# Performance work log

Hardware: AMD Instinct MI355X
Metric: run time of the kernel (lower is better)

The kernel has to match this reference:

```python
import jax, jax.numpy as jnp
import numpy as np

BOOST_STRENGTH = 1.0  # init kwarg boostStrength (already >= 0)


def setup_inputs() -> dict:
    key = jax.random.key(0)
    k1, k2 = jax.random.split(key)
    x = jax.random.normal(k1, (8192, 4096), dtype=jnp.float32)
    # duty cycles are running fractions of activity, roughly around k/n
    dutyCycles = jax.random.uniform(k2, (4096,), dtype=jnp.float32) * 0.2
    return {"x": x, "dutyCycles": dutyCycles, "k": 409}


def reference(x, dutyCycles, k):
    n = x.shape[1]
    boost_strength = jnp.maximum(jnp.float32(BOOST_STRENGTH), 0.0)
    target_density = jnp.float32(k) / jnp.float32(n)
    # boostFactors = exp[(targetDensity - dutyCycle) * boostStrength]
    boost_factors = jnp.exp((target_density - dutyCycles) * boost_strength)  # [n]
    boosted = x * boost_factors  # [B, n]
    topk_vals, _ = jax.lax.top_k(boosted, k)  # [B, k]
    bottom = jnp.min(topk_vals, axis=1, keepdims=True)  # per-row k-th largest
    mask = (boosted >= bottom).astype(x.dtype)
    return x * mask
```

## Files before the change

### kernel.cpp

```cpp
#include <hip/hip_runtime.h>
#include <cstdint>
#include <cstddef>

#define N_COLS 4096
#define TPB 256
#define NCOPY 8
#define HSTR 12
#define NHWORDS (256 * HSTR)
#define SURV_CAP 64

__global__ void boost_kernel(const float* __restrict__ dc,
                             const int* __restrict__ kp,
                             float* __restrict__ bf) {
    int i = blockIdx.x * blockDim.x + threadIdx.x;
    if (i < N_COLS) {
        float td = (float)kp[0] / (float)N_COLS;
        float arg = td - dc[i];
        bf[i] = (float)exp((double)arg);
    }
}

__device__ __forceinline__ uint32_t orderable(uint32_t u) {
    return (u & 0x80000000u) ? ~u : (u | 0x80000000u);
}

__global__ __launch_bounds__(TPB) void kwinner_kernel(
    const float* __restrict__ x, const float* __restrict__ bf,
    const int* __restrict__ kp, float* __restrict__ out)
{
    __shared__ uint32_t s_hist[NHWORDS];
    __shared__ uint32_t s_cnt[256];
    __shared__ uint32_t s_cand[SURV_CAP];
    __shared__ uint32_t s_m2;

    const int tid  = threadIdx.x;
    const int lane = tid & 63;
    const uint32_t copy = (uint32_t)(tid & (NCOPY - 1));
    const size_t row = blockIdx.x;
    const float4* xr = (const float4*)(x + row * (size_t)N_COLS);
    const float4* br = (const float4*)bf;
    float4* orow = (float4*)(out + row * (size_t)N_COLS);

    float4 xv[4];
    float xb[16];
    #pragma unroll
    for (int j = 0; j < 4; ++j) {
        float4 v = xr[tid + j * TPB];
        float4 b = br[tid + j * TPB];
        xv[j] = v;
        xb[j * 4 + 0] = v.x * b.x;
        xb[j * 4 + 1] = v.y * b.y;
        xb[j * 4 + 2] = v.z * b.z;
        xb[j * 4 + 3] = v.w * b.w;
    }

    {
        uint4* h4 = (uint4*)s_hist;
        uint4 z; z.x = z.y = z.z = z.w = 0u;
        #pragma unroll
        for (int j = 0; j < 3; ++j) h4[tid + j * TPB] = z;
    }
    if (tid == 0) s_m2 = 0;
    __syncthreads();

    const float T0f = 1.10f;
    #pragma unroll
    for (int e = 0; e < 16; ++e) {
        if (xb[e] >= T0f) {
            uint32_t d = (__float_as_uint(xb[e]) >> 16) - 0x3F80u;
            d = d > 255u ? 255u : d;
            atomicAdd(&s_hist[d * HSTR + copy], 1u);
        }
    }
    __syncthreads();

    const uint32_t k = (uint32_t)kp[0];
    uint32_t rem = k;

    uint32_t dsel;
    uint32_t packed;
    {
        uint32_t vv[4];
        const uint32_t b0 = (uint32_t)lane * 4u;
        #pragma unroll
        for (int i = 0; i < 4; ++i) {
            uint4 a  = *(const uint4*)&s_hist[(b0 + i) * HSTR];
            uint4 b2 = *(const uint4*)&s_hist[(b0 + i) * HSTR + 4];
            vv[i] = a.x + a.y + a.z + a.w + b2.x + b2.y + b2.z + b2.w;
        }
        uint32_t s3 = vv[3], s2 = vv[2] + s3, s1 = vv[1] + s2, s0 = vv[0] + s1;
        uint32_t T = s0;
        #pragma unroll
        for (int off = 1; off < 64; off <<= 1) {
            uint32_t t = (uint32_t)__shfl_down((int)T, off, 64);
            if (lane + off < 64) T += t;
        }
        uint32_t Tex = T - s0;
        uint32_t S0 = Tex + s0, S1 = Tex + s1, S2 = Tex + s2, S3 = Tex + s3;
        int b = -1; uint32_t sn = 0;
        if (S3 >= rem)      { b = 3; sn = S3 - vv[3]; }
        else if (S2 >= rem) { b = 2; sn = S2 - vv[2]; }
        else if (S1 >= rem) { b = 1; sn = S1 - vv[1]; }
        else if (S0 >= rem) { b = 0; sn = S0 - vv[0]; }
        packed = (b >= 0) ? ((((uint32_t)(4 * lane + b + 1)) << 16) | sn) : 0u;
        #pragma unroll
        for (int off = 1; off < 64; off <<= 1) {
            uint32_t o = (uint32_t)__shfl_xor((int)packed, off, 64);
            packed = packed > o ? packed : o;
        }
        dsel = (packed >> 16) - 1u;
        rem -= (packed & 0xFFFFu);
    }

    float thr = 0.0f;
    bool need_fallback = (packed == 0u) || (dsel == 255u);

    if (!need_fallback) {
        const uint32_t hi16 = 0x3F80u + dsel;
        #pragma unroll
        for (int e = 0; e < 16; ++e) {
            uint32_t ub = __float_as_uint(xb[e]);
            if ((ub >> 16) == hi16) {
                uint32_t pos = atomicAdd(&s_m2, 1u);
                if (pos < SURV_CAP) s_cand[pos] = ub;
            }
        }
        __syncthreads();
        const uint32_t m2 = s_m2;
        if (m2 <= SURV_CAP) {
            uint32_t cv = ((uint32_t)lane < m2) ? s_cand[lane] : ((~hi16) << 16);
            uint32_t cur = 0;
            #pragma unroll
            for (int bpos = 15; bpos >= 0; --bpos) {
                uint32_t t  = (hi16 << 16) | cur | (1u << bpos);
                uint32_t mk = ~((1u << bpos) - 1u);
                uint32_t c  = (uint32_t)__popcll(__ballot(((cv ^ t) & mk) == 0u));
                if (c >= rem) cur |= (1u << bpos);
                else          rem -= c;
            }
            thr = __uint_as_float((hi16 << 16) | cur);
        } else {
            need_fallback = true;
        }
    }

    if (need_fallback) {
        __syncthreads();
        {
            uint4* h4 = (uint4*)s_hist;
            uint4 z; z.x = z.y = z.z = z.w = 0u;
            #pragma unroll
            for (int j = 0; j < 3; ++j) h4[tid + j * TPB] = z;
        }
        __syncthreads();
        uint32_t prefix = 0;
        rem = k;
        const uint32_t pmasks[4] = {0u, 0xFF000000u, 0xFFFF0000u, 0xFFFFFF00u};
        #pragma unroll 1
        for (int pass = 0; pass < 4; ++pass) {
            const int shift = 24 - pass * 8;
            const uint32_t pm = pmasks[pass];
            #pragma unroll
            for (int e = 0; e < 16; ++e) {
                uint32_t ou = orderable(__float_as_uint(xb[e]));
                if (((ou ^ prefix) & pm) == 0u)
                    atomicAdd(&s_hist[((ou >> shift) & 255u) * HSTR + copy], 1u);
            }
            __syncthreads();
            {
                uint4 a  = *(const uint4*)&s_hist[tid * HSTR];
                uint4 b2 = *(const uint4*)&s_hist[tid * HSTR + 4];
                uint4 z; z.x = z.y = z.z = z.w = 0u;
                *(uint4*)&s_hist[tid * HSTR]     = z;
                *(uint4*)&s_hist[tid * HSTR + 4] = z;
                s_cnt[tid] = a.x + a.y + a.z + a.w + b2.x + b2.y + b2.z + b2.w;
            }
            __syncthreads();
            uint4 v = ((const uint4*)s_cnt)[lane];
            uint32_t s3 = v.w, s2 = v.z + s3, s1 = v.y + s2, s0 = v.x + s1;
            uint32_t T = s0;
            #pragma unroll
            for (int off = 1; off < 64; off <<= 1) {
                uint32_t t = (uint32_t)__shfl_down((int)T, off, 64);
                if (lane + off < 64) T += t;
            }
            uint32_t Tex = T - s0;
            uint32_t S0 = Tex + s0, S1 = Tex + s1, S2 = Tex + s2, S3 = Tex + s3;
            int b = -1; uint32_t sn = 0;
            if (S3 >= rem)      { b = 3; sn = S3 - v.w; }
            else if (S2 >= rem) { b = 2; sn = S2 - v.z; }
            else if (S1 >= rem) { b = 1; sn = S1 - v.y; }
            else if (S0 >= rem) { b = 0; sn = S0 - v.x; }
            uint32_t pk = (b >= 0) ? ((((uint32_t)(4 * lane + b + 1)) << 16) | sn) : 0u;
            #pragma unroll
            for (int off = 1; off < 64; off <<= 1) {
                uint32_t o = (uint32_t)__shfl_xor((int)pk, off, 64);
                pk = pk > o ? pk : o;
            }
            prefix |= ((pk >> 16) - 1u) << shift;
            rem -= (pk & 0xFFFFu);
        }
        uint32_t tu = (prefix & 0x80000000u) ? (prefix & 0x7FFFFFFFu) : ~prefix;
        thr = __uint_as_float(tu);
    }

    #pragma unroll
    for (int j = 0; j < 4; ++j) {
        float4 o;
        o.x = (xb[j * 4 + 0] >= thr) ? xv[j].x : 0.0f;
        o.y = (xb[j * 4 + 1] >= thr) ? xv[j].y : 0.0f;
        o.z = (xb[j * 4 + 2] >= thr) ? xv[j].z : 0.0f;
        o.w = (xb[j * 4 + 3] >= thr) ? xv[j].w : 0.0f;
        orow[tid + j * TPB] = o;
    }
}

extern "C" void kernel_launch(void* const* d_in, const int* in_sizes, int n_in,
                              void* d_out, int out_size, void* d_ws, size_t ws_size,
                              hipStream_t stream) {
    const float* x  = (const float*)d_in[0];
    const float* dc = (const float*)d_in[1];
    const int*   kp = (const int*)d_in[2];
    float* out = (float*)d_out;
    float* bf  = (float*)d_ws;

    const int n    = in_sizes[1];
    const int rows = in_sizes[0] / n;

    boost_kernel<<<(n + TPB - 1) / TPB, TPB, 0, stream>>>(dc, kp, bf);
    kwinner_kernel<<<rows, TPB, 0, stream>>>(x, bf, kp, out);
}
```

Baseline: 231.2 us.

## Process four rows per block with next-row prefetch and copy-major histogram

Each block now handles four rows and loads the next row's data into registers while the current row is being selected, so global load latency overlaps the histogram and scan work. The boost factors are loaded once per block and reused across its rows. The histogram layout changes from bin-major to copy-major with a padded stride, which changes the LDS access pattern for the reduction. Barriers become explicit lgkmcnt waits plus s_barrier. The cost is fewer blocks (2048 instead of 8192) and higher register pressure from the double-buffered rows.

```diff
diff --git a/kernel.cpp b/kernel.cpp
--- a/kernel.cpp
+++ b/kernel.cpp
@@ -4,10 +4,13 @@
 
 #define N_COLS 4096
 #define TPB 256
+#define RPB 4
 #define NCOPY 8
-#define HSTR 12
-#define NHWORDS (256 * HSTR)
+#define CSTR 260
+#define NHWORDS (NCOPY * CSTR)
 #define SURV_CAP 64
+
+static_assert(NHWORDS % 4 == 0, "hist must be uint4-clearable");
 
 __global__ void boost_kernel(const float* __restrict__ dc,
                              const int* __restrict__ kp,
@@ -24,44 +27,40 @@
     return (u & 0x80000000u) ? ~u : (u | 0x80000000u);
 }
 
-__global__ __launch_bounds__(TPB) void kwinner_kernel(
-    const float* __restrict__ x, const float* __restrict__ bf,
-    const int* __restrict__ kp, float* __restrict__ out)
+__device__ __forceinline__ void bar_lgkm() {
+    asm volatile("s_waitcnt lgkmcnt(0)\n\ts_barrier" ::: "memory");
+}
+
+template<bool PREF>
+__device__ __forceinline__ void process_row(
+    const float4* __restrict__ xpref, float4 (&xv)[4], float4 (&xn)[4],
+    const float4 (&bfv)[4], float4* __restrict__ orow, uint32_t k,
+    uint32_t* __restrict__ s_hist, uint32_t* __restrict__ s_cnt,
+    uint32_t* __restrict__ s_cand, uint32_t* __restrict__ s_m2,
+    int tid, int lane, uint32_t copy)
 {
-    __shared__ uint32_t s_hist[NHWORDS];
-    __shared__ uint32_t s_cnt[256];
-    __shared__ uint32_t s_cand[SURV_CAP];
-    __shared__ uint32_t s_m2;
-
-    const int tid  = threadIdx.x;
-    const int lane = tid & 63;
-    const uint32_t copy = (uint32_t)(tid & (NCOPY - 1));
-    const size_t row = blockIdx.x;
-    const float4* xr = (const float4*)(x + row * (size_t)N_COLS);
-    const float4* br = (const float4*)bf;
-    float4* orow = (float4*)(out + row * (size_t)N_COLS);
-
-    float4 xv[4];
-    float xb[16];
-    #pragma unroll
-    for (int j = 0; j < 4; ++j) {
-        float4 v = xr[tid + j * TPB];
-        float4 b = br[tid + j * TPB];
-        xv[j] = v;
-        xb[j * 4 + 0] = v.x * b.x;
-        xb[j * 4 + 1] = v.y * b.y;
-        xb[j * 4 + 2] = v.z * b.z;
-        xb[j * 4 + 3] = v.w * b.w;
-    }
-
+    if constexpr (PREF) {
+        #pragma unroll
+        for (int j = 0; j < 4; ++j) xn[j] = xpref[tid + j * TPB];
+    }
+
+    bar_lgkm();
     {
         uint4* h4 = (uint4*)s_hist;
         uint4 z; z.x = z.y = z.z = z.w = 0u;
-        #pragma unroll
-        for (int j = 0; j < 3; ++j) h4[tid + j * TPB] = z;
-    }
-    if (tid == 0) s_m2 = 0;
-    __syncthreads();
+        for (int w = tid; w < NHWORDS / 4; w += TPB) h4[w] = z;
+    }
+    if (tid == 0) *s_m2 = 0u;
+    bar_lgkm();
+
+    float xb[16];
+    #pragma unroll
+    for (int j = 0; j < 4; ++j) {
+        xb[j * 4 + 0] = xv[j].x * bfv[j].x;
+        xb[j * 4 + 1] = xv[j].y * bfv[j].y;
+        xb[j * 4 + 2] = xv[j].z * bfv[j].z;
+        xb[j * 4 + 3] = xv[j].w * bfv[j].w;
+    }
 
     const float T0f = 1.10f;
     #pragma unroll
@@ -69,26 +68,21 @@
         if (xb[e] >= T0f) {
             uint32_t d = (__float_as_uint(xb[e]) >> 16) - 0x3F80u;
             d = d > 255u ? 255u : d;
-            atomicAdd(&s_hist[d * HSTR + copy], 1u);
-        }
-    }
-    __syncthreads();
-
-    const uint32_t k = (uint32_t)kp[0];
+            atomicAdd(&s_hist[copy * CSTR + d], 1u);
+        }
+    }
+    bar_lgkm();
+
     uint32_t rem = k;
-
-    uint32_t dsel;
-    uint32_t packed;
+    uint32_t dsel, packed;
     {
-        uint32_t vv[4];
-        const uint32_t b0 = (uint32_t)lane * 4u;
-        #pragma unroll
-        for (int i = 0; i < 4; ++i) {
-            uint4 a  = *(const uint4*)&s_hist[(b0 + i) * HSTR];
-            uint4 b2 = *(const uint4*)&s_hist[(b0 + i) * HSTR + 4];
-            vv[i] = a.x + a.y + a.z + a.w + b2.x + b2.y + b2.z + b2.w;
-        }
-        uint32_t s3 = vv[3], s2 = vv[2] + s3, s1 = vv[1] + s2, s0 = vv[0] + s1;
+        uint32_t vv0 = 0, vv1 = 0, vv2 = 0, vv3 = 0;
+        #pragma unroll
+        for (int c = 0; c < NCOPY; ++c) {
+            uint4 a = *(const uint4*)&s_hist[c * CSTR + 4 * lane];
+            vv0 += a.x; vv1 += a.y; vv2 += a.z; vv3 += a.w;
+        }
+        uint32_t s3 = vv3, s2 = vv2 + s3, s1 = vv1 + s2, s0 = vv0 + s1;
         uint32_t T = s0;
         #pragma unroll
         for (int off = 1; off < 64; off <<= 1) {
@@ -98,10 +92,10 @@
         uint32_t Tex = T - s0;
         uint32_t S0 = Tex + s0, S1 = Tex + s1, S2 = Tex + s2, S3 = Tex + s3;
         int b = -1; uint32_t sn = 0;
-        if (S3 >= rem)      { b = 3; sn = S3 - vv[3]; }
-        else if (S2 >= rem) { b = 2; sn = S2 - vv[2]; }
-        else if (S1 >= rem) { b = 1; sn = S1 - vv[1]; }
-        else if (S0 >= rem) { b = 0; sn = S0 - vv[0]; }
+        if (S3 >= rem)      { b = 3; sn = S3 - vv3; }
+        else if (S2 >= rem) { b = 2; sn = S2 - vv2; }
+        else if (S1 >= rem) { b = 1; sn = S1 - vv1; }
+        else if (S0 >= rem) { b = 0; sn = S0 - vv0; }
         packed = (b >= 0) ? ((((uint32_t)(4 * lane + b + 1)) << 16) | sn) : 0u;
         #pragma unroll
         for (int off = 1; off < 64; off <<= 1) {
@@ -121,12 +115,12 @@
         for (int e = 0; e < 16; ++e) {
             uint32_t ub = __float_as_uint(xb[e]);
             if ((ub >> 16) == hi16) {
-                uint32_t pos = atomicAdd(&s_m2, 1u);
+                uint32_t pos = atomicAdd(s_m2, 1u);
                 if (pos < SURV_CAP) s_cand[pos] = ub;
             }
         }
-        __syncthreads();
-        const uint32_t m2 = s_m2;
+        bar_lgkm();
+        const uint32_t m2 = *s_m2;
         if (m2 <= SURV_CAP) {
             uint32_t cv = ((uint32_t)lane < m2) ? s_cand[lane] : ((~hi16) << 16);
             uint32_t cur = 0;
@@ -145,14 +139,13 @@
     }
 
     if (need_fallback) {
-        __syncthreads();
+        bar_lgkm();
         {
             uint4* h4 = (uint4*)s_hist;
             uint4 z; z.x = z.y = z.z = z.w = 0u;
-            #pragma unroll
-            for (int j = 0; j < 3; ++j) h4[tid + j * TPB] = z;
-        }
-        __syncthreads();
+            for (int w = tid; w < NHWORDS / 4; w += TPB) h4[w] = z;
+        }
+        bar_lgkm();
         uint32_t prefix = 0;
         rem = k;
         const uint32_t pmasks[4] = {0u, 0xFF000000u, 0xFFFF0000u, 0xFFFFFF00u};
@@ -164,18 +157,19 @@
             for (int e = 0; e < 16; ++e) {
                 uint32_t ou = orderable(__float_as_uint(xb[e]));
                 if (((ou ^ prefix) & pm) == 0u)
-                    atomicAdd(&s_hist[((ou >> shift) & 255u) * HSTR + copy], 1u);
-            }
-            __syncthreads();
+                    atomicAdd(&s_hist[copy * CSTR + ((ou >> shift) & 255u)], 1u);
+            }
+            bar_lgkm();
             {
-                uint4 a  = *(const uint4*)&s_hist[tid * HSTR];
-                uint4 b2 = *(const uint4*)&s_hist[tid * HSTR + 4];
-                uint4 z; z.x = z.y = z.z = z.w = 0u;
-                *(uint4*)&s_hist[tid * HSTR]     = z;
-                *(uint4*)&s_hist[tid * HSTR + 4] = z;
-                s_cnt[tid] = a.x + a.y + a.z + a.w + b2.x + b2.y + b2.z + b2.w;
-            }
-            __syncthreads();
+                uint32_t sum = 0;
+                #pragma unroll
+                for (int c = 0; c < NCOPY; ++c) {
+                    sum += s_hist[c * CSTR + tid];
+                    s_hist[c * CSTR + tid] = 0u;
+                }
+                s_cnt[tid] = sum;
+            }
+            bar_lgkm();
             uint4 v = ((const uint4*)s_cnt)[lane];
             uint32_t s3 = v.w, s2 = v.z + s3, s1 = v.y + s2, s0 = v.x + s1;
             uint32_t T = s0;
@@ -215,6 +209,51 @@
     }
 }
 
+__global__ __launch_bounds__(TPB) void kwinner_kernel(
+    const float* __restrict__ x, const float* __restrict__ bf,
+    const int* __restrict__ kp, float* __restrict__ out, int rows)
+{
+    __shared__ __align__(16) uint32_t s_hist[NHWORDS];
+    __shared__ uint32_t s_cnt[256];
+    __shared__ uint32_t s_cand[SURV_CAP];
+    __shared__ uint32_t s_m2;
+
+    const int tid  = threadIdx.x;
+    const int lane = tid & 63;
+    const uint32_t copy = (uint32_t)(tid & (NCOPY - 1));
+    const uint32_t k = (uint32_t)kp[0];
+
+    size_t r0 = (size_t)blockIdx.x * RPB;
+    size_t r1 = r0 + 1, r2 = r0 + 2, r3 = r0 + 3;
+    const size_t rmax = (size_t)rows - 1;
+    if (r0 > rmax) r0 = rmax;
+    if (r1 > rmax) r1 = rmax;
+    if (r2 > rmax) r2 = rmax;
+    if (r3 > rmax) r3 = rmax;
+
+    const float4* br = (const float4*)bf;
+    float4 bfv[4];
+    #pragma unroll
+    for (int j = 0; j < 4; ++j) bfv[j] = br[tid + j * TPB];
+
+    const size_t s4 = N_COLS / 4;
+    const float4* xg = (const float4*)x;
+    float4* og = (float4*)out;
+
+    float4 xA[4], xB[4];
+    #pragma unroll
+    for (int j = 0; j < 4; ++j) xA[j] = xg[r0 * s4 + tid + j * TPB];
+
+    process_row<true >(xg + r1 * s4, xA, xB, bfv, og + r0 * s4, k,
+                       s_hist, s_cnt, s_cand, &s_m2, tid, lane, copy);
+    process_row<true >(xg + r2 * s4, xB, xA, bfv, og + r1 * s4, k,
+                       s_hist, s_cnt, s_cand, &s_m2, tid, lane, copy);
+    process_row<true >(xg + r3 * s4, xA, xB, bfv, og + r2 * s4, k,
+                       s_hist, s_cnt, s_cand, &s_m2, tid, lane, copy);
+    process_row<false>(xg,           xB, xA, bfv, og + r3 * s4, k,
+                       s_hist, s_cnt, s_cand, &s_m2, tid, lane, copy);
+}
+
 extern "C" void kernel_launch(void* const* d_in, const int* in_sizes, int n_in,
                               void* d_out, int out_size, void* d_ws, size_t ws_size,
                               hipStream_t stream) {
@@ -228,5 +267,6 @@
     const int rows = in_sizes[0] / n;
 
     boost_kernel<<<(n + TPB - 1) / TPB, TPB, 0, stream>>>(dc, kp, bf);
-    kwinner_kernel<<<rows, TPB, 0, stream>>>(x, bf, kp, out);
-}
+    const int nb = (rows + RPB - 1) / RPB;
+    kwinner_kernel<<<nb, TPB, 0, stream>>>(x, bf, kp, out, rows);
+}
```

Result: slower. 245.5 us (+6.2%).

## Process one row per wavefront with wave-local histograms and LDS-staged boost factors

Applied to the files above, without the earlier changes.

Each 64-lane wavefront now owns a whole row: 16 float4 per lane, a private two-copy histogram, and private candidate buffers. Block-wide __syncthreads are replaced by wave-local lgkmcnt waits. Boost factors are staged once per block in LDS and the boosted products are recomputed from it instead of being held in registers. This removes block barriers and cross-wave histogram reduction, at the cost of more registers per lane, more LDS atomic contention within a wave, and relying on wave-synchronous LDS ordering.

```diff
diff --git a/kernel.cpp b/kernel.cpp
--- a/kernel.cpp
+++ b/kernel.cpp
@@ -4,9 +4,8 @@
 
 #define N_COLS 4096
 #define TPB 256
-#define NCOPY 8
-#define HSTR 12
-#define NHWORDS (256 * HSTR)
+#define WPB 4
+#define HSTRW 260
 #define SURV_CAP 64
 
 __global__ void boost_kernel(const float* __restrict__ dc,
@@ -24,71 +23,77 @@
     return (u & 0x80000000u) ? ~u : (u | 0x80000000u);
 }
 
-__global__ __launch_bounds__(TPB) void kwinner_kernel(
+__device__ __forceinline__ void wave_lgkm() {
+    asm volatile("s_waitcnt lgkmcnt(0)" ::: "memory");
+}
+
+__global__ __launch_bounds__(TPB, 4) void kwinner_kernel(
     const float* __restrict__ x, const float* __restrict__ bf,
-    const int* __restrict__ kp, float* __restrict__ out)
+    const int* __restrict__ kp, float* __restrict__ out, int rows)
 {
-    __shared__ uint32_t s_hist[NHWORDS];
-    __shared__ uint32_t s_cnt[256];
-    __shared__ uint32_t s_cand[SURV_CAP];
-    __shared__ uint32_t s_m2;
+    __shared__ __align__(16) float    s_bf[N_COLS];
+    __shared__ __align__(16) uint32_t s_hist[WPB][2][HSTRW];
+    __shared__ uint32_t s_cand[WPB][SURV_CAP];
+    __shared__ uint32_t s_m2[WPB * 8];
 
     const int tid  = threadIdx.x;
+    const int w    = tid >> 6;
     const int lane = tid & 63;
-    const uint32_t copy = (uint32_t)(tid & (NCOPY - 1));
-    const size_t row = blockIdx.x;
-    const float4* xr = (const float4*)(x + row * (size_t)N_COLS);
-    const float4* br = (const float4*)bf;
-    float4* orow = (float4*)(out + row * (size_t)N_COLS);
-
-    float4 xv[4];
-    float xb[16];
+
+    {
+        const float4* br = (const float4*)bf;
+        float4* sb = (float4*)s_bf;
+        #pragma unroll
+        for (int j = 0; j < 4; ++j) sb[tid + j * TPB] = br[tid + j * TPB];
+    }
+    __syncthreads();
+
+    size_t row = (size_t)blockIdx.x * WPB + (size_t)w;
+    const size_t rmax = (size_t)rows - 1;
+    if (row > rmax) row = rmax;
+
+    const float4* xr   = (const float4*)(x + row * (size_t)N_COLS);
+    float4*       orow = (float4*)(out + row * (size_t)N_COLS);
+    const float4* bf4  = (const float4*)s_bf;
+
+    float4 xv[16];
     #pragma unroll
-    for (int j = 0; j < 4; ++j) {
-        float4 v = xr[tid + j * TPB];
-        float4 b = br[tid + j * TPB];
-        xv[j] = v;
-        xb[j * 4 + 0] = v.x * b.x;
-        xb[j * 4 + 1] = v.y * b.y;
-        xb[j * 4 + 2] = v.z * b.z;
-        xb[j * 4 + 3] = v.w * b.w;
-    }
+    for (int jj = 0; jj < 16; ++jj) xv[jj] = xr[lane + 64 * jj];
+
+    uint32_t* hist = &s_hist[w][0][0];
+    uint32_t* m2p  = &s_m2[w * 8];
 
     {
-        uint4* h4 = (uint4*)s_hist;
         uint4 z; z.x = z.y = z.z = z.w = 0u;
-        #pragma unroll
-        for (int j = 0; j < 3; ++j) h4[tid + j * TPB] = z;
-    }
-    if (tid == 0) s_m2 = 0;
-    __syncthreads();
-
+        *(uint4*)&hist[4 * lane]         = z;
+        *(uint4*)&hist[HSTRW + 4 * lane] = z;
+        if (lane == 0) *m2p = 0u;
+    }
+    wave_lgkm();
+
+    const uint32_t cofs = (uint32_t)(lane & 1) * HSTRW;
     const float T0f = 1.10f;
     #pragma unroll
-    for (int e = 0; e < 16; ++e) {
-        if (xb[e] >= T0f) {
-            uint32_t d = (__float_as_uint(xb[e]) >> 16) - 0x3F80u;
-            d = d > 255u ? 255u : d;
-            atomicAdd(&s_hist[d * HSTR + copy], 1u);
-        }
-    }
-    __syncthreads();
+    for (int jj = 0; jj < 16; ++jj) {
+        float4 b = bf4[lane + 64 * jj];
+        float xb0 = xv[jj].x * b.x, xb1 = xv[jj].y * b.y;
+        float xb2 = xv[jj].z * b.z, xb3 = xv[jj].w * b.w;
+        if (xb0 >= T0f) { uint32_t d = (__float_as_uint(xb0) >> 16) - 0x3F80u; d = d > 255u ? 255u : d; atomicAdd(&hist[cofs + d], 1u); }
+        if (xb1 >= T0f) { uint32_t d = (__float_as_uint(xb1) >> 16) - 0x3F80u; d = d > 255u ? 255u : d; atomicAdd(&hist[cofs + d], 1u); }
+        if (xb2 >= T0f) { uint32_t d = (__float_as_uint(xb2) >> 16) - 0x3F80u; d = d > 255u ? 255u : d; atomicAdd(&hist[cofs + d], 1u); }
+        if (xb3 >= T0f) { uint32_t d = (__float_as_uint(xb3) >> 16) - 0x3F80u; d = d > 255u ? 255u : d; atomicAdd(&hist[cofs + d], 1u); }
+    }
+    wave_lgkm();
 
     const uint32_t k = (uint32_t)kp[0];
     uint32_t rem = k;
 
-    uint32_t dsel;
-    uint32_t packed;
+    uint32_t dsel, packed;
     {
-        uint32_t vv[4];
-        const uint32_t b0 = (uint32_t)lane * 4u;
-        #pragma unroll
-        for (int i = 0; i < 4; ++i) {
-            uint4 a  = *(const uint4*)&s_hist[(b0 + i) * HSTR];
-            uint4 b2 = *(const uint4*)&s_hist[(b0 + i) * HSTR + 4];
-            vv[i] = a.x + a.y + a.z + a.w + b2.x + b2.y + b2.z + b2.w;
-        }
-        uint32_t s3 = vv[3], s2 = vv[2] + s3, s1 = vv[1] + s2, s0 = vv[0] + s1;
+        uint4 a  = *(const uint4*)&hist[4 * lane];
+        uint4 b2 = *(const uint4*)&hist[HSTRW + 4 * lane];
+        uint32_t vv0 = a.x + b2.x, vv1 = a.y + b2.y, vv2 = a.z + b2.z, vv3 = a.w + b2.w;
+        uint32_t s3 = vv3, s2 = vv2 + s3, s1 = vv1 + s2, s0 = vv0 + s1;
         uint32_t T = s0;
         #pragma unroll
         for (int off = 1; off < 64; off <<= 1) {
@@ -98,10 +103,10 @@
         uint32_t Tex = T - s0;
         uint32_t S0 = Tex + s0, S1 = Tex + s1, S2 = Tex + s2, S3 = Tex + s3;
         int b = -1; uint32_t sn = 0;
-        if (S3 >= rem)      { b = 3; sn = S3 - vv[3]; }
-        else if (S2 >= rem) { b = 2; sn = S2 - vv[2]; }
-        else if (S1 >= rem) { b = 1; sn = S1 - vv[1]; }
-        else if (S0 >= rem) { b = 0; sn = S0 - vv[0]; }
+        if (S3 >= rem)      { b = 3; sn = S3 - vv3; }
+        else if (S2 >= rem) { b = 2; sn = S2 - vv2; }
+        else if (S1 >= rem) { b = 1; sn = S1 - vv1; }
+        else if (S0 >= rem) { b = 0; sn = S0 - vv0; }
         packed = (b >= 0) ? ((((uint32_t)(4 * lane + b + 1)) << 16) | sn) : 0u;
         #pragma unroll
         for (int off = 1; off < 64; off <<= 1) {
@@ -118,17 +123,21 @@
     if (!need_fallback) {
         const uint32_t hi16 = 0x3F80u + dsel;
         #pragma unroll
-        for (int e = 0; e < 16; ++e) {
-            uint32_t ub = __float_as_uint(xb[e]);
-            if ((ub >> 16) == hi16) {
-                uint32_t pos = atomicAdd(&s_m2, 1u);
-                if (pos < SURV_CAP) s_cand[pos] = ub;
-            }
-        }
-        __syncthreads();
-        const uint32_t m2 = s_m2;
+        for (int jj = 0; jj < 16; ++jj) {
+            float4 b = bf4[lane + 64 * jj];
+            float xb0 = xv[jj].x * b.x, xb1 = xv[jj].y * b.y;
+            float xb2 = xv[jj].z * b.z, xb3 = xv[jj].w * b.w;
+            uint32_t u0 = __float_as_uint(xb0), u1 = __float_as_uint(xb1);
+            uint32_t u2 = __float_as_uint(xb2), u3 = __float_as_uint(xb3);
+            if ((u0 >> 16) == hi16) { uint32_t p = atomicAdd(m2p, 1u); if (p < SURV_CAP) s_cand[w][p] = u0; }
+            if ((u1 >> 16) == hi16) { uint32_t p = atomicAdd(m2p, 1u); if (p < SURV_CAP) s_cand[w][p] = u1; }
+            if ((u2 >> 16) == hi16) { uint32_t p = atomicAdd(m2p, 1u); if (p < SURV_CAP) s_cand[w][p] = u2; }
+            if ((u3 >> 16) == hi16) { uint32_t p = atomicAdd(m2p, 1u); if (p < SURV_CAP) s_cand[w][p] = u3; }
+        }
+        wave_lgkm();
+        const uint32_t m2 = *m2p;
         if (m2 <= SURV_CAP) {
-            uint32_t cv = ((uint32_t)lane < m2) ? s_cand[lane] : ((~hi16) << 16);
+            uint32_t cv = ((uint32_t)lane < m2) ? s_cand[w][lane] : ((~hi16) << 16);
             uint32_t cur = 0;
             #pragma unroll
             for (int bpos = 15; bpos >= 0; --bpos) {
@@ -145,14 +154,12 @@
     }
 
     if (need_fallback) {
-        __syncthreads();
         {
-            uint4* h4 = (uint4*)s_hist;
             uint4 z; z.x = z.y = z.z = z.w = 0u;
-            #pragma unroll
-            for (int j = 0; j < 3; ++j) h4[tid + j * TPB] = z;
-        }
-        __syncthreads();
+            *(uint4*)&hist[4 * lane]         = z;
+            *(uint4*)&hist[HSTRW + 4 * lane] = z;
+        }
+        wave_lgkm();
         uint32_t prefix = 0;
         rem = k;
         const uint32_t pmasks[4] = {0u, 0xFF000000u, 0xFFFF0000u, 0xFFFFFF00u};
@@ -161,23 +168,31 @@
             const int shift = 24 - pass * 8;
             const uint32_t pm = pmasks[pass];
             #pragma unroll
-            for (int e = 0; e < 16; ++e) {
-                uint32_t ou = orderable(__float_as_uint(xb[e]));
-                if (((ou ^ prefix) & pm) == 0u)
-                    atomicAdd(&s_hist[((ou >> shift) & 255u) * HSTR + copy], 1u);
-            }
-            __syncthreads();
+            for (int jj = 0; jj < 16; ++jj) {
+                float4 b = bf4[lane + 64 * jj];
+                float xb0 = xv[jj].x * b.x, xb1 = xv[jj].y * b.y;
+                float xb2 = xv[jj].z * b.z, xb3 = xv[jj].w * b.w;
+                uint32_t ou;
+                ou = orderable(__float_as_uint(xb0));
+                if (((ou ^ prefix) & pm) == 0u) atomicAdd(&hist[cofs + ((ou >> shift) & 255u)], 1u);
+                ou = orderable(__float_as_uint(xb1));
+                if (((ou ^ prefix) & pm) == 0u) atomicAdd(&hist[cofs + ((ou >> shift) & 255u)], 1u);
+                ou = orderable(__float_as_uint(xb2));
+                if (((ou ^ prefix) & pm) == 0u) atomicAdd(&hist[cofs + ((ou >> shift) & 255u)], 1u);
+                ou = orderable(__float_as_uint(xb3));
+                if (((ou ^ prefix) & pm) == 0u) atomicAdd(&hist[cofs + ((ou >> shift) & 255u)], 1u);
+            }
+            wave_lgkm();
+            uint4 a  = *(const uint4*)&hist[4 * lane];
+            uint4 b2 = *(const uint4*)&hist[HSTRW + 4 * lane];
             {
-                uint4 a  = *(const uint4*)&s_hist[tid * HSTR];
-                uint4 b2 = *(const uint4*)&s_hist[tid * HSTR + 4];
                 uint4 z; z.x = z.y = z.z = z.w = 0u;
-                *(uint4*)&s_hist[tid * HSTR]     = z;
-                *(uint4*)&s_hist[tid * HSTR + 4] = z;
-                s_cnt[tid] = a.x + a.y + a.z + a.w + b2.x + b2.y + b2.z + b2.w;
-            }
-            __syncthreads();
-            uint4 v = ((const uint4*)s_cnt)[lane];
-            uint32_t s3 = v.w, s2 = v.z + s3, s1 = v.y + s2, s0 = v.x + s1;
+                *(uint4*)&hist[4 * lane]         = z;
+                *(uint4*)&hist[HSTRW + 4 * lane] = z;
+            }
+            wave_lgkm();
+            uint32_t vv0 = a.x + b2.x, vv1 = a.y + b2.y, vv2 = a.z + b2.z, vv3 = a.w + b2.w;
+            uint32_t s3 = vv3, s2 = vv2 + s3, s1 = vv1 + s2, s0 = vv0 + s1;
             uint32_t T = s0;
             #pragma unroll
             for (int off = 1; off < 64; off <<= 1) {
@@ -187,10 +202,10 @@
             uint32_t Tex = T - s0;
             uint32_t S0 = Tex + s0, S1 = Tex + s1, S2 = Tex + s2, S3 = Tex + s3;
             int b = -1; uint32_t sn = 0;
-            if (S3 >= rem)      { b = 3; sn = S3 - v.w; }
-            else if (S2 >= rem) { b = 2; sn = S2 - v.z; }
-            else if (S1 >= rem) { b = 1; sn = S1 - v.y; }
-            else if (S0 >= rem) { b = 0; sn = S0 - v.x; }
+            if (S3 >= rem)      { b = 3; sn = S3 - vv3; }
+            else if (S2 >= rem) { b = 2; sn = S2 - vv2; }
+            else if (S1 >= rem) { b = 1; sn = S1 - vv1; }
+            else if (S0 >= rem) { b = 0; sn = S0 - vv0; }
             uint32_t pk = (b >= 0) ? ((((uint32_t)(4 * lane + b + 1)) << 16) | sn) : 0u;
             #pragma unroll
             for (int off = 1; off < 64; off <<= 1) {
@@ -205,13 +220,14 @@
     }
 
     #pragma unroll
-    for (int j = 0; j < 4; ++j) {
+    for (int jj = 0; jj < 16; ++jj) {
+        float4 b = bf4[lane + 64 * jj];
         float4 o;
-        o.x = (xb[j * 4 + 0] >= thr) ? xv[j].x : 0.0f;
-        o.y = (xb[j * 4 + 1] >= thr) ? xv[j].y : 0.0f;
-        o.z = (xb[j * 4 + 2] >= thr) ? xv[j].z : 0.0f;
-        o.w = (xb[j * 4 + 3] >= thr) ? xv[j].w : 0.0f;
-        orow[tid + j * TPB] = o;
+        o.x = (xv[jj].x * b.x >= thr) ? xv[jj].x : 0.0f;
+        o.y = (xv[jj].y * b.y >= thr) ? xv[jj].y : 0.0f;
+        o.z = (xv[jj].z * b.z >= thr) ? xv[jj].z : 0.0f;
+        o.w = (xv[jj].w * b.w >= thr) ? xv[jj].w : 0.0f;
+        orow[lane + 64 * jj] = o;
     }
 }
 
@@ -228,5 +244,6 @@
     const int rows = in_sizes[0] / n;
 
     boost_kernel<<<(n + TPB - 1) / TPB, TPB, 0, stream>>>(dc, kp, bf);
-    kwinner_kernel<<<rows, TPB, 0, stream>>>(x, bf, kp, out);
-}
+    const int nb = (rows + WPB - 1) / WPB;
+    kwinner_kernel<<<nb, TPB, 0, stream>>>(x, bf, kp, out, rows);
+}
```

Result: slower. 242.9 us (+5.1%).

## Process two rows per block with per-wave histograms and interleaved selection

Applied to the files above, without the earlier changes.

Each block now handles two rows, sharing the boost-factor loads and running the histogram scan, shuffle reductions and ballot refinement for both rows interleaved, which gives more independent work per wave to hide latency. Histogram copies move from a thread-strided layout to one copy per wave (4 copies), which cuts the per-bin reduction cost but adds more atomic contention. The x rows are re-read from global memory before the output write instead of being kept in registers, trading extra load traffic for lower register pressure. The fallback radix select is moved into a helper function.

```diff
diff --git a/kernel.cpp b/kernel.cpp
--- a/kernel.cpp
+++ b/kernel.cpp
@@ -4,9 +4,10 @@
 
 #define N_COLS 4096
 #define TPB 256
-#define NCOPY 8
-#define HSTR 12
-#define NHWORDS (256 * HSTR)
+#define RPB 2
+#define NCOPY 4
+#define CSTR 260
+#define HWORDS (NCOPY * CSTR)
 #define SURV_CAP 64
 
 __global__ void boost_kernel(const float* __restrict__ dc,
@@ -24,71 +25,44 @@
     return (u & 0x80000000u) ? ~u : (u | 0x80000000u);
 }
 
-__global__ __launch_bounds__(TPB) void kwinner_kernel(
-    const float* __restrict__ x, const float* __restrict__ bf,
-    const int* __restrict__ kp, float* __restrict__ out)
+__device__ __forceinline__ float radix_select(const float (&xb)[16],
+    uint32_t* __restrict__ hist, int w, int lane, int tid, uint32_t k)
 {
-    __shared__ uint32_t s_hist[NHWORDS];
-    __shared__ uint32_t s_cnt[256];
-    __shared__ uint32_t s_cand[SURV_CAP];
-    __shared__ uint32_t s_m2;
-
-    const int tid  = threadIdx.x;
-    const int lane = tid & 63;
-    const uint32_t copy = (uint32_t)(tid & (NCOPY - 1));
-    const size_t row = blockIdx.x;
-    const float4* xr = (const float4*)(x + row * (size_t)N_COLS);
-    const float4* br = (const float4*)bf;
-    float4* orow = (float4*)(out + row * (size_t)N_COLS);
-
-    float4 xv[4];
-    float xb[16];
-    #pragma unroll
-    for (int j = 0; j < 4; ++j) {
-        float4 v = xr[tid + j * TPB];
-        float4 b = br[tid + j * TPB];
-        xv[j] = v;
-        xb[j * 4 + 0] = v.x * b.x;
-        xb[j * 4 + 1] = v.y * b.y;
-        xb[j * 4 + 2] = v.z * b.z;
-        xb[j * 4 + 3] = v.w * b.w;
-    }
-
     {
-        uint4* h4 = (uint4*)s_hist;
+        uint4* h4 = (uint4*)hist;
         uint4 z; z.x = z.y = z.z = z.w = 0u;
         #pragma unroll
-        for (int j = 0; j < 3; ++j) h4[tid + j * TPB] = z;
-    }
-    if (tid == 0) s_m2 = 0;
+        for (int i = 0; i < 2; ++i) { int idx = tid + i * TPB; if (idx < HWORDS / 4) h4[idx] = z; }
+    }
     __syncthreads();
-
-    const float T0f = 1.10f;
-    #pragma unroll
-    for (int e = 0; e < 16; ++e) {
-        if (xb[e] >= T0f) {
-            uint32_t d = (__float_as_uint(xb[e]) >> 16) - 0x3F80u;
-            d = d > 255u ? 255u : d;
-            atomicAdd(&s_hist[d * HSTR + copy], 1u);
-        }
-    }
-    __syncthreads();
-
-    const uint32_t k = (uint32_t)kp[0];
-    uint32_t rem = k;
-
-    uint32_t dsel;
-    uint32_t packed;
-    {
-        uint32_t vv[4];
-        const uint32_t b0 = (uint32_t)lane * 4u;
-        #pragma unroll
-        for (int i = 0; i < 4; ++i) {
-            uint4 a  = *(const uint4*)&s_hist[(b0 + i) * HSTR];
-            uint4 b2 = *(const uint4*)&s_hist[(b0 + i) * HSTR + 4];
-            vv[i] = a.x + a.y + a.z + a.w + b2.x + b2.y + b2.z + b2.w;
-        }
-        uint32_t s3 = vv[3], s2 = vv[2] + s3, s1 = vv[1] + s2, s0 = vv[0] + s1;
+    uint32_t* hc = hist + (size_t)w * CSTR;
+    uint32_t prefix = 0, rem = k;
+    const uint32_t pmasks[4] = {0u, 0xFF000000u, 0xFFFF0000u, 0xFFFFFF00u};
+    #pragma unroll 1
+    for (int pass = 0; pass < 4; ++pass) {
+        const int shift = 24 - pass * 8;
+        const uint32_t pm = pmasks[pass];
+        #pragma unroll
+        for (int e = 0; e < 16; ++e) {
+            uint32_t ou = orderable(__float_as_uint(xb[e]));
+            if (((ou ^ prefix) & pm) == 0u) atomicAdd(&hc[(ou >> shift) & 255u], 1u);
+        }
+        __syncthreads();
+        uint32_t v0 = 0, v1 = 0, v2 = 0, v3 = 0;
+        #pragma unroll
+        for (int c = 0; c < NCOPY; ++c) {
+            uint4 a = *(const uint4*)&hist[c * CSTR + 4 * lane];
+            v0 += a.x; v1 += a.y; v2 += a.z; v3 += a.w;
+        }
+        __syncthreads();
+        {
+            uint4* h4 = (uint4*)hist;
+            uint4 z; z.x = z.y = z.z = z.w = 0u;
+            #pragma unroll
+            for (int i = 0; i < 2; ++i) { int idx = tid + i * TPB; if (idx < HWORDS / 4) h4[idx] = z; }
+        }
+        __syncthreads();
+        uint32_t s3 = v3, s2 = v2 + s3, s1 = v1 + s2, s0 = v0 + s1;
         uint32_t T = s0;
         #pragma unroll
         for (int off = 1; off < 64; off <<= 1) {
@@ -98,120 +72,215 @@
         uint32_t Tex = T - s0;
         uint32_t S0 = Tex + s0, S1 = Tex + s1, S2 = Tex + s2, S3 = Tex + s3;
         int b = -1; uint32_t sn = 0;
-        if (S3 >= rem)      { b = 3; sn = S3 - vv[3]; }
-        else if (S2 >= rem) { b = 2; sn = S2 - vv[2]; }
-        else if (S1 >= rem) { b = 1; sn = S1 - vv[1]; }
-        else if (S0 >= rem) { b = 0; sn = S0 - vv[0]; }
-        packed = (b >= 0) ? ((((uint32_t)(4 * lane + b + 1)) << 16) | sn) : 0u;
+        if (S3 >= rem)      { b = 3; sn = S3 - v3; }
+        else if (S2 >= rem) { b = 2; sn = S2 - v2; }
+        else if (S1 >= rem) { b = 1; sn = S1 - v1; }
+        else if (S0 >= rem) { b = 0; sn = S0 - v0; }
+        uint32_t pk = (b >= 0) ? ((((uint32_t)(4 * lane + b + 1)) << 16) | sn) : 0u;
         #pragma unroll
         for (int off = 1; off < 64; off <<= 1) {
-            uint32_t o = (uint32_t)__shfl_xor((int)packed, off, 64);
-            packed = packed > o ? packed : o;
-        }
-        dsel = (packed >> 16) - 1u;
-        rem -= (packed & 0xFFFFu);
-    }
-
-    float thr = 0.0f;
-    bool need_fallback = (packed == 0u) || (dsel == 255u);
-
-    if (!need_fallback) {
-        const uint32_t hi16 = 0x3F80u + dsel;
+            uint32_t o = (uint32_t)__shfl_xor((int)pk, off, 64);
+            pk = pk > o ? pk : o;
+        }
+        prefix |= ((pk >> 16) - 1u) << shift;
+        rem -= (pk & 0xFFFFu);
+    }
+    uint32_t tu = (prefix & 0x80000000u) ? (prefix & 0x7FFFFFFFu) : ~prefix;
+    return __uint_as_float(tu);
+}
+
+__global__ __launch_bounds__(TPB) void kwinner_kernel(
+    const float* __restrict__ x, const float* __restrict__ bf,
+    const int* __restrict__ kp, float* __restrict__ out, int rows)
+{
+    __shared__ __align__(16) uint32_t s_hist[RPB][NCOPY][CSTR];
+    __shared__ uint32_t s_cand[RPB][SURV_CAP];
+    __shared__ uint32_t s_m2[RPB * 8];
+
+    const int tid  = threadIdx.x;
+    const int lane = tid & 63;
+    const int w    = tid >> 6;
+
+    size_t rA = (size_t)blockIdx.x * RPB;
+    size_t rB = rA + 1;
+    const size_t rmax = (size_t)rows - 1;
+    if (rA > rmax) rA = rmax;
+    if (rB > rmax) rB = rmax;
+
+    const float4* xrA = (const float4*)(x + rA * (size_t)N_COLS);
+    const float4* xrB = (const float4*)(x + rB * (size_t)N_COLS);
+    float4* oA = (float4*)(out + rA * (size_t)N_COLS);
+    float4* oB = (float4*)(out + rB * (size_t)N_COLS);
+    const float4* bfr = (const float4*)bf;
+
+    float4 xa[4], xc[4], bb[4];
+    #pragma unroll
+    for (int j = 0; j < 4; ++j) xa[j] = xrA[tid + j * TPB];
+    #pragma unroll
+    for (int j = 0; j < 4; ++j) xc[j] = xrB[tid + j * TPB];
+    #pragma unroll
+    for (int j = 0; j < 4; ++j) bb[j] = bfr[tid + j * TPB];
+
+    float xbA[16], xbB[16];
+    #pragma unroll
+    for (int j = 0; j < 4; ++j) {
+        xbA[4 * j + 0] = xa[j].x * bb[j].x;  xbA[4 * j + 1] = xa[j].y * bb[j].y;
+        xbA[4 * j + 2] = xa[j].z * bb[j].z;  xbA[4 * j + 3] = xa[j].w * bb[j].w;
+        xbB[4 * j + 0] = xc[j].x * bb[j].x;  xbB[4 * j + 1] = xc[j].y * bb[j].y;
+        xbB[4 * j + 2] = xc[j].z * bb[j].z;  xbB[4 * j + 3] = xc[j].w * bb[j].w;
+    }
+
+    {
+        uint4* h4 = (uint4*)&s_hist[0][0][0];
+        uint4 z; z.x = z.y = z.z = z.w = 0u;
+        #pragma unroll
+        for (int i = 0; i < 3; ++i) {
+            int idx = tid + i * TPB;
+            if (idx < (HWORDS * RPB) / 4) h4[idx] = z;
+        }
+        if (tid < RPB) s_m2[tid * 8] = 0u;
+    }
+    __syncthreads();
+
+    const float T0f = 1.10f;
+    uint32_t* hA = &s_hist[0][w][0];
+    uint32_t* hB = &s_hist[1][w][0];
+    #pragma unroll
+    for (int e = 0; e < 16; ++e) {
+        if (xbA[e] >= T0f) {
+            uint32_t d = (__float_as_uint(xbA[e]) >> 16) - 0x3F80u;
+            d = d > 255u ? 255u : d;
+            atomicAdd(&hA[d], 1u);
+        }
+        if (xbB[e] >= T0f) {
+            uint32_t d = (__float_as_uint(xbB[e]) >> 16) - 0x3F80u;
+            d = d > 255u ? 255u : d;
+            atomicAdd(&hB[d], 1u);
+        }
+    }
+    __syncthreads();
+
+    const uint32_t k = (uint32_t)kp[0];
+    uint32_t rem[2] = {k, k};
+    uint32_t packed[2], dsel[2];
+    {
+        uint32_t vv[2][4];
+        #pragma unroll
+        for (int r = 0; r < 2; ++r) {
+            uint32_t v0 = 0, v1 = 0, v2 = 0, v3 = 0;
+            #pragma unroll
+            for (int c = 0; c < NCOPY; ++c) {
+                uint4 a = *(const uint4*)&s_hist[r][c][4 * lane];
+                v0 += a.x; v1 += a.y; v2 += a.z; v3 += a.w;
+            }
+            vv[r][0] = v0; vv[r][1] = v1; vv[r][2] = v2; vv[r][3] = v3;
+        }
+        uint32_t s3[2], s2[2], s1[2], s0[2], T[2];
+        #pragma unroll
+        for (int r = 0; r < 2; ++r) {
+            s3[r] = vv[r][3]; s2[r] = vv[r][2] + s3[r];
+            s1[r] = vv[r][1] + s2[r]; s0[r] = vv[r][0] + s1[r];
+            T[r] = s0[r];
+        }
+        #pragma unroll
+        for (int off = 1; off < 64; off <<= 1) {
+            uint32_t tA = (uint32_t)__shfl_down((int)T[0], off, 64);
+            uint32_t tB = (uint32_t)__shfl_down((int)T[1], off, 64);
+            if (lane + off < 64) { T[0] += tA; T[1] += tB; }
+        }
+        #pragma unroll
+        for (int r = 0; r < 2; ++r) {
+            uint32_t Tex = T[r] - s0[r];
+            uint32_t S0 = Tex + s0[r], S1 = Tex + s1[r], S2 = Tex + s2[r], S3 = Tex + s3[r];
+            int b = -1; uint32_t sn = 0;
+            if (S3 >= rem[r])      { b = 3; sn = S3 - vv[r][3]; }
+            else if (S2 >= rem[r]) { b = 2; sn = S2 - vv[r][2]; }
+            else if (S1 >= rem[r]) { b = 1; sn = S1 - vv[r][1]; }
+            else if (S0 >= rem[r]) { b = 0; sn = S0 - vv[r][0]; }
+            packed[r] = (b >= 0) ? ((((uint32_t)(4 * lane + b + 1)) << 16) | sn) : 0u;
+        }
+        #pragma unroll
+        for (int off = 1; off < 64; off <<= 1) {
+            uint32_t oA = (uint32_t)__shfl_xor((int)packed[0], off, 64);
+            uint32_t oB = (uint32_t)__shfl_xor((int)packed[1], off, 64);
+            packed[0] = packed[0] > oA ? packed[0] : oA;
+            packed[1] = packed[1] > oB ? packed[1] : oB;
+        }
+        dsel[0] = (packed[0] >> 16) - 1u;  rem[0] -= (packed[0] & 0xFFFFu);
+        dsel[1] = (packed[1] >> 16) - 1u;  rem[1] -= (packed[1] & 0xFFFFu);
+    }
+
+    bool valid[2] = { packed[0] != 0u && dsel[0] != 255u,
+                      packed[1] != 0u && dsel[1] != 255u };
+    uint32_t hi16[2] = { 0x3F80u + dsel[0], 0x3F80u + dsel[1] };
+
+    if (valid[0]) {
         #pragma unroll
         for (int e = 0; e < 16; ++e) {
-            uint32_t ub = __float_as_uint(xb[e]);
-            if ((ub >> 16) == hi16) {
-                uint32_t pos = atomicAdd(&s_m2, 1u);
-                if (pos < SURV_CAP) s_cand[pos] = ub;
+            uint32_t ub = __float_as_uint(xbA[e]);
+            if ((ub >> 16) == hi16[0]) {
+                uint32_t p = atomicAdd(&s_m2[0], 1u);
+                if (p < SURV_CAP) s_cand[0][p] = ub;
             }
         }
-        __syncthreads();
-        const uint32_t m2 = s_m2;
-        if (m2 <= SURV_CAP) {
-            uint32_t cv = ((uint32_t)lane < m2) ? s_cand[lane] : ((~hi16) << 16);
-            uint32_t cur = 0;
-            #pragma unroll
-            for (int bpos = 15; bpos >= 0; --bpos) {
-                uint32_t t  = (hi16 << 16) | cur | (1u << bpos);
-                uint32_t mk = ~((1u << bpos) - 1u);
-                uint32_t c  = (uint32_t)__popcll(__ballot(((cv ^ t) & mk) == 0u));
-                if (c >= rem) cur |= (1u << bpos);
-                else          rem -= c;
+    }
+    if (valid[1]) {
+        #pragma unroll
+        for (int e = 0; e < 16; ++e) {
+            uint32_t ub = __float_as_uint(xbB[e]);
+            if ((ub >> 16) == hi16[1]) {
+                uint32_t p = atomicAdd(&s_m2[8], 1u);
+                if (p < SURV_CAP) s_cand[1][p] = ub;
             }
-            thr = __uint_as_float((hi16 << 16) | cur);
-        } else {
-            need_fallback = true;
-        }
-    }
-
-    if (need_fallback) {
-        __syncthreads();
-        {
-            uint4* h4 = (uint4*)s_hist;
-            uint4 z; z.x = z.y = z.z = z.w = 0u;
-            #pragma unroll
-            for (int j = 0; j < 3; ++j) h4[tid + j * TPB] = z;
-        }
-        __syncthreads();
-        uint32_t prefix = 0;
-        rem = k;
-        const uint32_t pmasks[4] = {0u, 0xFF000000u, 0xFFFF0000u, 0xFFFFFF00u};
-        #pragma unroll 1
-        for (int pass = 0; pass < 4; ++pass) {
-            const int shift = 24 - pass * 8;
-            const uint32_t pm = pmasks[pass];
-            #pragma unroll
-            for (int e = 0; e < 16; ++e) {
-                uint32_t ou = orderable(__float_as_uint(xb[e]));
-                if (((ou ^ prefix) & pm) == 0u)
-                    atomicAdd(&s_hist[((ou >> shift) & 255u) * HSTR + copy], 1u);
-            }
-            __syncthreads();
-            {
-                uint4 a  = *(const uint4*)&s_hist[tid * HSTR];
-                uint4 b2 = *(const uint4*)&s_hist[tid * HSTR + 4];
-                uint4 z; z.x = z.y = z.z = z.w = 0u;
-                *(uint4*)&s_hist[tid * HSTR]     = z;
-                *(uint4*)&s_hist[tid * HSTR + 4] = z;
-                s_cnt[tid] = a.x + a.y + a.z + a.w + b2.x + b2.y + b2.z + b2.w;
-            }
-            __syncthreads();
-            uint4 v = ((const uint4*)s_cnt)[lane];
-            uint32_t s3 = v.w, s2 = v.z + s3, s1 = v.y + s2, s0 = v.x + s1;
-            uint32_t T = s0;
-            #pragma unroll
-            for (int off = 1; off < 64; off <<= 1) {
-                uint32_t t = (uint32_t)__shfl_down((int)T, off, 64);
-                if (lane + off < 64) T += t;
-            }
-            uint32_t Tex = T - s0;
-            uint32_t S0 = Tex + s0, S1 = Tex + s1, S2 = Tex + s2, S3 = Tex + s3;
-            int b = -1; uint32_t sn = 0;
-            if (S3 >= rem)      { b = 3; sn = S3 - v.w; }
-            else if (S2 >= rem) { b = 2; sn = S2 - v.z; }
-            else if (S1 >= rem) { b = 1; sn = S1 - v.y; }
-            else if (S0 >= rem) { b = 0; sn = S0 - v.x; }
-            uint32_t pk = (b >= 0) ? ((((uint32_t)(4 * lane + b + 1)) << 16) | sn) : 0u;
-            #pragma unroll
-            for (int off = 1; off < 64; off <<= 1) {
-                uint32_t o = (uint32_t)__shfl_xor((int)pk, off, 64);
-                pk = pk > o ? pk : o;
-            }
-            prefix |= ((pk >> 16) - 1u) << shift;
-            rem -= (pk & 0xFFFFu);
-        }
-        uint32_t tu = (prefix & 0x80000000u) ? (prefix & 0x7FFFFFFFu) : ~prefix;
-        thr = __uint_as_float(tu);
-    }
-
+        }
+    }
+    __syncthreads();
+    uint32_t m2[2] = { s_m2[0], s_m2[8] };
+    if (m2[0] > SURV_CAP) valid[0] = false;
+    if (m2[1] > SURV_CAP) valid[1] = false;
+
+    float thr[2] = {0.0f, 0.0f};
+    {
+        uint32_t cv[2], cur[2] = {0u, 0u}, rr[2] = { rem[0], rem[1] };
+        #pragma unroll
+        for (int r = 0; r < 2; ++r)
+            cv[r] = (valid[r] && (uint32_t)lane < m2[r]) ? s_cand[r][lane]
+                                                         : ((~hi16[r]) << 16);
+        #pragma unroll
+        for (int bpos = 15; bpos >= 0; --bpos) {
+            uint32_t mk = ~((1u << bpos) - 1u);
+            uint32_t tA = (hi16[0] << 16) | cur[0] | (1u << bpos);
+            uint32_t tB = (hi16[1] << 16) | cur[1] | (1u << bpos);
+            uint32_t cA = (uint32_t)__popcll(__ballot(((cv[0] ^ tA) & mk) == 0u));
+            uint32_t cB = (uint32_t)__popcll(__ballot(((cv[1] ^ tB) & mk) == 0u));
+            if (cA >= rr[0]) cur[0] |= (1u << bpos); else rr[0] -= cA;
+            if (cB >= rr[1]) cur[1] |= (1u << bpos); else rr[1] -= cB;
+        }
+        if (valid[0]) thr[0] = __uint_as_float((hi16[0] << 16) | cur[0]);
+        if (valid[1]) thr[1] = __uint_as_float((hi16[1] << 16) | cur[1]);
+    }
+
+    if (!valid[0]) thr[0] = radix_select(xbA, &s_hist[0][0][0], w, lane, tid, k);
+    if (!valid[1]) thr[1] = radix_select(xbB, &s_hist[1][0][0], w, lane, tid, k);
+
+    #pragma unroll
+    for (int j = 0; j < 4; ++j) xa[j] = xrA[tid + j * TPB];
+    #pragma unroll
+    for (int j = 0; j < 4; ++j) xc[j] = xrB[tid + j * TPB];
     #pragma unroll
     for (int j = 0; j < 4; ++j) {
         float4 o;
-        o.x = (xb[j * 4 + 0] >= thr) ? xv[j].x : 0.0f;
-        o.y = (xb[j * 4 + 1] >= thr) ? xv[j].y : 0.0f;
-        o.z = (xb[j * 4 + 2] >= thr) ? xv[j].z : 0.0f;
-        o.w = (xb[j * 4 + 3] >= thr) ? xv[j].w : 0.0f;
-        orow[tid + j * TPB] = o;
+        o.x = (xbA[4 * j + 0] >= thr[0]) ? xa[j].x : 0.0f;
+        o.y = (xbA[4 * j + 1] >= thr[0]) ? xa[j].y : 0.0f;
+        o.z = (xbA[4 * j + 2] >= thr[0]) ? xa[j].z : 0.0f;
+        o.w = (xbA[4 * j + 3] >= thr[0]) ? xa[j].w : 0.0f;
+        oA[tid + j * TPB] = o;
+        float4 p;
+        p.x = (xbB[4 * j + 0] >= thr[1]) ? xc[j].x : 0.0f;
+        p.y = (xbB[4 * j + 1] >= thr[1]) ? xc[j].y : 0.0f;
+        p.z = (xbB[4 * j + 2] >= thr[1]) ? xc[j].z : 0.0f;
+        p.w = (xbB[4 * j + 3] >= thr[1]) ? xc[j].w : 0.0f;
+        oB[tid + j * TPB] = p;
     }
 }
 
@@ -228,5 +297,6 @@
     const int rows = in_sizes[0] / n;
 
     boost_kernel<<<(n + TPB - 1) / TPB, TPB, 0, stream>>>(dc, kp, bf);
-    kwinner_kernel<<<rows, TPB, 0, stream>>>(x, bf, kp, out);
-}
+    const int nb = (rows + RPB - 1) / RPB;
+    kwinner_kernel<<<nb, TPB, 0, stream>>>(x, bf, kp, out, rows);
+}
```

After: 238.7 us. 3.3% more time.
